# Optimization experiments

Hardware: AMD Instinct MI355X
Metric: run time of the kernel (lower is better)

Reference implementation:

```python
import jax, jax.numpy as jnp
import numpy as np

B, S, T, D = 64, 50, 200, 128
IN2, H = 128, 64
NEG = -1e10


def setup_inputs() -> dict:
    key = jax.random.key(0)
    k1, k2, k3, k4, k5, k6, k7, k8 = jax.random.split(key, 8)
    inp = jax.random.normal(k1, (B, S, T, D), dtype=jnp.float32)
    z = jax.random.normal(k2, (B, S, IN2), dtype=jnp.float32)
    mask = jax.random.randint(k3, (B, S, T), 0, 2, dtype=jnp.int32)
    # torch nn.Linear weights: [out, in]
    W1 = jax.random.normal(k4, (H, D), dtype=jnp.float32) / np.sqrt(D)
    W2_w = jax.random.normal(k5, (H, IN2), dtype=jnp.float32) / np.sqrt(IN2)
    W2_b = jax.random.normal(k6, (H,), dtype=jnp.float32) * 0.01
    V_w = jax.random.normal(k7, (1, H), dtype=jnp.float32) / np.sqrt(H)
    V_b = jax.random.normal(k8, (1,), dtype=jnp.float32) * 0.01
    return {"input": inp, "z": z, "mask": mask, "W1": W1,
            "W2_w": W2_w, "W2_b": W2_b, "V_w": V_w, "V_b": V_b}


def reference(input, z, mask, W1, W2_w, W2_b, V_w, V_b):
    # w1h: [B,S,T,H]
    w1h = jnp.einsum('bstd,hd->bsth', input, W1)
    # w2h: [B,S,H] (Linear with bias), broadcast over T
    w2h = jnp.einsum('bsd,hd->bsh', z, W2_w) + W2_b
    u = jnp.tanh(w1h + w2h[:, :, None, :])           # [B,S,T,H]
    att = jnp.einsum('bsth,h->bst', u, V_w[0]) + V_b[0]  # [B,S,T]
    att = jnp.where(mask == 0, NEG, att)
    att = jax.nn.softmax(att, axis=2)
    out = jnp.einsum('bst,bstd->bsd', att, input)    # [B,S,D]
    return out
```

## Files before the change

kernel.cpp:

```cpp
#include <hip/hip_runtime.h>

#define Tdim 200
#define Ddim 128
#define Hdim 64
#define NBS  3200
#define NEGV (-1e10f)

typedef _Float16 f16x8 __attribute__((ext_vector_type(8)));
typedef float    floatx4 __attribute__((ext_vector_type(4)));

__device__ __forceinline__ unsigned int packf16(float a, float b) {
    _Float16 ha = (_Float16)a, hb = (_Float16)b;
    unsigned int ua = *(unsigned short*)&ha, ub = *(unsigned short*)&hb;
    return ua | (ub << 16);
}

__device__ __forceinline__ float ftanh(float x) {
    float e = __expf(2.0f * x);
    return 1.0f - 2.0f * __builtin_amdgcn_rcpf(e + 1.0f);
}

__global__ __launch_bounds__(256, 3) void attn_main(
    const float* __restrict__ X, const float* __restrict__ z,
    const int* __restrict__ mask,
    const float* __restrict__ W1, const float* __restrict__ W2w,
    const float* __restrict__ W2b,
    const float* __restrict__ Vw, const float* __restrict__ Vb,
    float* __restrict__ out)
{
    __shared__ __align__(16) unsigned short xs[Tdim * 128];
    __shared__ float attL[Tdim];
    __shared__ float red[8];
    __shared__ float pp[256];
    __shared__ float w2hL[Hdim];

    const int tid = threadIdx.x;
    const int bs  = blockIdx.x;
    const float* __restrict__ Xb = X + (size_t)bs * (Tdim * Ddim);

    #pragma unroll 5
    for (int it = 0; it < 25; ++it) {
        int j = it * 256 + tid;
        int t = j >> 5, dq = j & 31;
        float4 v = *(const float4*)(Xb + t * Ddim + dq * 4);
        unsigned int lo = packf16(v.x, v.y);
        unsigned int hi = packf16(v.z, v.w);
        int u16 = t * 16 + ((dq >> 1) ^ (t & 15));
        *(uint2*)((char*)xs + u16 * 16 + (dq & 1) * 8) = make_uint2(lo, hi);
    }

    const int lane = tid & 63;
    const int wv   = tid >> 6;
    const int l15  = lane & 15, quad = lane >> 4;

    f16x8 bfrag[4][4];
    #pragma unroll
    for (int n = 0; n < 4; ++n)
        #pragma unroll
        for (int ks = 0; ks < 4; ++ks) {
            const float* wp = W1 + (n * 16 + l15) * 128 + ks * 32 + quad * 8;
            float4 v0 = *(const float4*)wp;
            float4 v1 = *(const float4*)(wp + 4);
            uint4 u = make_uint4(packf16(v0.x, v0.y), packf16(v0.z, v0.w),
                                 packf16(v1.x, v1.y), packf16(v1.z, v1.w));
            bfrag[n][ks] = *(f16x8*)&u;
        }

    {
        const int h = tid >> 2, q = tid & 3;
        const float4* zp = (const float4*)(z + (size_t)bs * 128 + q * 32);
        const float4* wp = (const float4*)(W2w + h * 128 + q * 32);
        float a = 0.f;
        #pragma unroll
        for (int i = 0; i < 8; ++i) {
            float4 zv = zp[i], wv4 = wp[i];
            a = fmaf(zv.x, wv4.x, a); a = fmaf(zv.y, wv4.y, a);
            a = fmaf(zv.z, wv4.z, a); a = fmaf(zv.w, wv4.w, a);
        }
        a += __shfl_xor(a, 1);
        a += __shfl_xor(a, 2);
        if (q == 0) w2hL[h] = a + W2b[h];
    }

    const float Vb0 = Vb[0];
    float vw[4];
    #pragma unroll
    for (int n = 0; n < 4; ++n) vw[n] = Vw[l15 + 16 * n];

    __syncthreads();

    float w2[4];
    #pragma unroll
    for (int n = 0; n < 4; ++n) w2[n] = w2hL[l15 + 16 * n];

    for (int mt = wv; mt < 13; mt += 4) {
        const int t0 = (mt == 12) ? 184 : mt * 16;
        const int trow = t0 + l15;
        floatx4 acc[4];
        #pragma unroll
        for (int n = 0; n < 4; ++n) acc[n] = (floatx4){0.f, 0.f, 0.f, 0.f};
        f16x8 afrag[4];
        #pragma unroll
        for (int ks = 0; ks < 4; ++ks) {
            int u16 = trow * 16 + (((ks << 2) + quad) ^ (trow & 15));
            afrag[ks] = *(const f16x8*)(xs + u16 * 8);
        }
        #pragma unroll
        for (int n = 0; n < 4; ++n)
            #pragma unroll
            for (int ks = 0; ks < 4; ++ks)
                acc[n] = __builtin_amdgcn_mfma_f32_16x16x32_f16(afrag[ks], bfrag[n][ks], acc[n], 0, 0, 0);

        float s0 = 0.f, s1 = 0.f, s2 = 0.f, s3 = 0.f;
        #pragma unroll
        for (int n = 0; n < 4; ++n) {
            s0 = fmaf(ftanh(acc[n][0] + w2[n]), vw[n], s0);
            s1 = fmaf(ftanh(acc[n][1] + w2[n]), vw[n], s1);
            s2 = fmaf(ftanh(acc[n][2] + w2[n]), vw[n], s2);
            s3 = fmaf(ftanh(acc[n][3] + w2[n]), vw[n], s3);
        }
        #pragma unroll
        for (int m = 1; m < 16; m <<= 1) {
            s0 += __shfl_xor(s0, m);
            s1 += __shfl_xor(s1, m);
            s2 += __shfl_xor(s2, m);
            s3 += __shfl_xor(s3, m);
        }
        if (l15 == 0) {
            const int tb = t0 + quad * 4;
            attL[tb]     = s0 + Vb0;
            attL[tb + 1] = s1 + Vb0;
            attL[tb + 2] = s2 + Vb0;
            attL[tb + 3] = s3 + Vb0;
        }
    }
    __syncthreads();

    float l = -3e38f;
    if (tid < Tdim) {
        l = attL[tid];
        if (mask[bs * Tdim + tid] == 0) l = NEGV;
    }
    float m = l;
    #pragma unroll
    for (int off = 32; off > 0; off >>= 1) m = fmaxf(m, __shfl_xor(m, off));
    if (lane == 0) red[wv] = m;
    __syncthreads();
    const float M = fmaxf(fmaxf(red[0], red[1]), fmaxf(red[2], red[3]));
    float p = __expf(l - M);
    float sm = p;
    #pragma unroll
    for (int off = 32; off > 0; off >>= 1) sm += __shfl_xor(sm, off);
    if (lane == 0) red[4 + wv] = sm;
    __syncthreads();
    const float S = (red[4] + red[5]) + (red[6] + red[7]);
    if (tid < Tdim) attL[tid] = p / S;
    __syncthreads();

    const int d = tid & 127, half = tid >> 7;
    const _Float16* xsh = (const _Float16*)xs;
    const int d3 = d >> 3, dl = d & 7;
    float o = 0.f;
    #pragma unroll 4
    for (int tt = 0; tt < 100; ++tt) {
        int t = half * 100 + tt;
        int idx = t * 128 + ((d3 ^ (t & 15)) << 3) + dl;
        o = fmaf(attL[t], (float)xsh[idx], o);
    }
    pp[tid] = o;
    __syncthreads();
    if (tid < 128) out[bs * Ddim + tid] = pp[tid] + pp[tid + 128];
}

extern "C" void kernel_launch(void* const* d_in, const int* in_sizes, int n_in,
                              void* d_out, int out_size, void* d_ws, size_t ws_size,
                              hipStream_t stream) {
    const float* X    = (const float*)d_in[0];
    const float* z    = (const float*)d_in[1];
    const int*   mask = (const int*)d_in[2];
    const float* W1   = (const float*)d_in[3];
    const float* W2w  = (const float*)d_in[4];
    const float* W2b  = (const float*)d_in[5];
    const float* Vw   = (const float*)d_in[6];
    const float* Vb   = (const float*)d_in[7];
    float* out = (float*)d_out;

    attn_main<<<NBS, 256, 0, stream>>>(X, z, mask, W1, W2w, W2b, Vw, Vb, out);
}
```

Measured before the change: 490.3 us.

## Give each wave its own X rows so MFMA starts without a block barrier

Each wave now converts and stores into shared memory only the rows it will later use for its MFMA tiles. This removes the block-wide barrier between loading X and computing scores, so a wave can start its math as soon as its own rows are in place. The W2 projection is computed and synchronised before the load, and the mask value is fetched early into a register. The final attention-weighted sum now reads 8 halves per shared-memory access and reduces with shuffles, dropping the pp buffer and one barrier. In exchange, wave 3 carries more rows and one more tile than the others, and correctness relies on ordering of shared-memory writes and reads within a single wave.

New measurement: 473.7 us. 3.4% less time.

```diff
diff --git a/kernel.cpp b/kernel.cpp
--- a/kernel.cpp
+++ b/kernel.cpp
@@ -31,27 +31,47 @@
     __shared__ __align__(16) unsigned short xs[Tdim * 128];
     __shared__ float attL[Tdim];
     __shared__ float red[8];
-    __shared__ float pp[256];
     __shared__ float w2hL[Hdim];
 
     const int tid = threadIdx.x;
     const int bs  = blockIdx.x;
     const float* __restrict__ Xb = X + (size_t)bs * (Tdim * Ddim);
-
-    #pragma unroll 5
-    for (int it = 0; it < 25; ++it) {
-        int j = it * 256 + tid;
-        int t = j >> 5, dq = j & 31;
+    const int lane = tid & 63;
+    const int wv   = tid >> 6;
+    const int l15  = lane & 15, quad = lane >> 4;
+
+    int mval = 1;
+    if (tid < Tdim) mval = mask[bs * Tdim + tid];
+
+    {
+        const int h = tid >> 2, q = tid & 3;
+        const float4* zp = (const float4*)(z + (size_t)bs * 128 + q * 32);
+        const float4* wp = (const float4*)(W2w + h * 128 + q * 32);
+        float a = 0.f;
+        #pragma unroll
+        for (int i = 0; i < 8; ++i) {
+            float4 zv = zp[i], wv4 = wp[i];
+            a = fmaf(zv.x, wv4.x, a); a = fmaf(zv.y, wv4.y, a);
+            a = fmaf(zv.z, wv4.z, a); a = fmaf(zv.w, wv4.w, a);
+        }
+        a += __shfl_xor(a, 1);
+        a += __shfl_xor(a, 2);
+        if (q == 0) w2hL[h] = a + W2b[h];
+    }
+    __syncthreads();
+
+    const int R0  = wv * 48;
+    const int nIt = (wv == 3) ? 28 : 24;
+    #pragma unroll 4
+    for (int i = 0; i < nIt; ++i) {
+        int j = i * 64 + lane;
+        int t = R0 + (j >> 5), dq = j & 31;
         float4 v = *(const float4*)(Xb + t * Ddim + dq * 4);
         unsigned int lo = packf16(v.x, v.y);
         unsigned int hi = packf16(v.z, v.w);
         int u16 = t * 16 + ((dq >> 1) ^ (t & 15));
         *(uint2*)((char*)xs + u16 * 16 + (dq & 1) * 8) = make_uint2(lo, hi);
     }
-
-    const int lane = tid & 63;
-    const int wv   = tid >> 6;
-    const int l15  = lane & 15, quad = lane >> 4;
 
     f16x8 bfrag[4][4];
     #pragma unroll
@@ -66,34 +86,16 @@
             bfrag[n][ks] = *(f16x8*)&u;
         }
 
-    {
-        const int h = tid >> 2, q = tid & 3;
-        const float4* zp = (const float4*)(z + (size_t)bs * 128 + q * 32);
-        const float4* wp = (const float4*)(W2w + h * 128 + q * 32);
-        float a = 0.f;
-        #pragma unroll
-        for (int i = 0; i < 8; ++i) {
-            float4 zv = zp[i], wv4 = wp[i];
-            a = fmaf(zv.x, wv4.x, a); a = fmaf(zv.y, wv4.y, a);
-            a = fmaf(zv.z, wv4.z, a); a = fmaf(zv.w, wv4.w, a);
-        }
-        a += __shfl_xor(a, 1);
-        a += __shfl_xor(a, 2);
-        if (q == 0) w2hL[h] = a + W2b[h];
-    }
-
     const float Vb0 = Vb[0];
-    float vw[4];
-    #pragma unroll
-    for (int n = 0; n < 4; ++n) vw[n] = Vw[l15 + 16 * n];
-
-    __syncthreads();
-
-    float w2[4];
-    #pragma unroll
-    for (int n = 0; n < 4; ++n) w2[n] = w2hL[l15 + 16 * n];
-
-    for (int mt = wv; mt < 13; mt += 4) {
+    float vwr[4], w2[4];
+    #pragma unroll
+    for (int n = 0; n < 4; ++n) {
+        vwr[n] = Vw[l15 + 16 * n];
+        w2[n]  = w2hL[l15 + 16 * n];
+    }
+
+    const int mtEnd = (wv == 3) ? 13 : wv * 3 + 3;
+    for (int mt = wv * 3; mt < mtEnd; ++mt) {
         const int t0 = (mt == 12) ? 184 : mt * 16;
         const int trow = t0 + l15;
         floatx4 acc[4];
@@ -114,10 +116,10 @@
         float s0 = 0.f, s1 = 0.f, s2 = 0.f, s3 = 0.f;
         #pragma unroll
         for (int n = 0; n < 4; ++n) {
-            s0 = fmaf(ftanh(acc[n][0] + w2[n]), vw[n], s0);
-            s1 = fmaf(ftanh(acc[n][1] + w2[n]), vw[n], s1);
-            s2 = fmaf(ftanh(acc[n][2] + w2[n]), vw[n], s2);
-            s3 = fmaf(ftanh(acc[n][3] + w2[n]), vw[n], s3);
+            s0 = fmaf(ftanh(acc[n][0] + w2[n]), vwr[n], s0);
+            s1 = fmaf(ftanh(acc[n][1] + w2[n]), vwr[n], s1);
+            s2 = fmaf(ftanh(acc[n][2] + w2[n]), vwr[n], s2);
+            s3 = fmaf(ftanh(acc[n][3] + w2[n]), vwr[n], s3);
         }
         #pragma unroll
         for (int m = 1; m < 16; m <<= 1) {
@@ -139,7 +141,7 @@
     float l = -3e38f;
     if (tid < Tdim) {
         l = attL[tid];
-        if (mask[bs * Tdim + tid] == 0) l = NEGV;
+        if (mval == 0) l = NEGV;
     }
     float m = l;
     #pragma unroll
@@ -157,19 +159,37 @@
     if (tid < Tdim) attL[tid] = p / S;
     __syncthreads();
 
-    const int d = tid & 127, half = tid >> 7;
-    const _Float16* xsh = (const _Float16*)xs;
-    const int d3 = d >> 3, dl = d & 7;
-    float o = 0.f;
-    #pragma unroll 4
-    for (int tt = 0; tt < 100; ++tt) {
-        int t = half * 100 + tt;
-        int idx = t * 128 + ((d3 ^ (t & 15)) << 3) + dl;
-        o = fmaf(attL[t], (float)xsh[idx], o);
-    }
-    pp[tid] = o;
-    __syncthreads();
-    if (tid < 128) out[bs * Ddim + tid] = pp[tid] + pp[tid + 128];
+    {
+        const int dblk = 4 * wv + (lane & 3);
+        const int tg   = lane >> 2;
+        float o0=0.f,o1=0.f,o2=0.f,o3=0.f,o4=0.f,o5=0.f,o6=0.f,o7=0.f;
+        #pragma unroll 4
+        for (int t = tg; t < Tdim; t += 16) {
+            int u16 = t * 16 + (dblk ^ (t & 15));
+            f16x8 xv = *(const f16x8*)(xs + u16 * 8);
+            float a = attL[t];
+            o0 = fmaf((float)xv[0], a, o0);
+            o1 = fmaf((float)xv[1], a, o1);
+            o2 = fmaf((float)xv[2], a, o2);
+            o3 = fmaf((float)xv[3], a, o3);
+            o4 = fmaf((float)xv[4], a, o4);
+            o5 = fmaf((float)xv[5], a, o5);
+            o6 = fmaf((float)xv[6], a, o6);
+            o7 = fmaf((float)xv[7], a, o7);
+        }
+        #pragma unroll
+        for (int m2 = 4; m2 <= 32; m2 <<= 1) {
+            o0 += __shfl_xor(o0, m2); o1 += __shfl_xor(o1, m2);
+            o2 += __shfl_xor(o2, m2); o3 += __shfl_xor(o3, m2);
+            o4 += __shfl_xor(o4, m2); o5 += __shfl_xor(o5, m2);
+            o6 += __shfl_xor(o6, m2); o7 += __shfl_xor(o7, m2);
+        }
+        if (tg == 0) {
+            float* op = out + bs * Ddim + dblk * 8;
+            *(float4*)op       = make_float4(o0, o1, o2, o3);
+            *(float4*)(op + 4) = make_float4(o4, o5, o6, o7);
+        }
+    }
 }
 
 extern "C" void kernel_launch(void* const* d_in, const int* in_sizes, int n_in,
```
